# Kernel optimization log

Hardware: AMD Instinct MI355X
Metric: run time of the kernel (lower is better)

Reference implementation:

```python
import jax, jax.numpy as jnp
import numpy as np

B, H, W = 16, 256, 256
C = 64          # width
M1, M2 = 12, 12 # retained Fourier modes
FC_HID = 128


def setup_inputs() -> dict:
    key = jax.random.key(0)
    ks = jax.random.split(key, 10)
    scale = 1.0 / (C * C)
    inp = {
        "x": jax.random.normal(ks[0], (B, H, W, 1), dtype=jnp.float32),
        "fc0_w": jax.random.normal(ks[1], (1, C), dtype=jnp.float32) * (1.0 / np.sqrt(1)),
        "fc0_b": jnp.zeros((C,), dtype=jnp.float32),
        # 4 layers x {weights1, weights2} x [Cin, Cout, M1, M2] x {re, im}
        "sc_w": jax.random.uniform(ks[2], (4, 2, C, C, M1, M2, 2), dtype=jnp.float32) * scale,
        # 1x1 conv weights [layer, Cout, Cin] and biases [layer, Cout]
        "pw_w": jax.random.normal(ks[3], (4, C, C), dtype=jnp.float32) * (1.0 / np.sqrt(C)),
        "pw_b": jnp.zeros((4, C), dtype=jnp.float32),
        "fc1_w": jax.random.normal(ks[4], (C, FC_HID), dtype=jnp.float32) * (1.0 / np.sqrt(C)),
        "fc1_b": jnp.zeros((FC_HID,), dtype=jnp.float32),
        "fc2_w": jax.random.normal(ks[5], (FC_HID, 1), dtype=jnp.float32) * (1.0 / np.sqrt(FC_HID)),
        "fc2_b": jnp.zeros((1,), dtype=jnp.float32),
    }
    return inp


def _spectral_conv(x, w1, w2):
    # x: [B, C, H, W] real; w1, w2: [Cin, Cout, M1, M2] complex
    xf = jnp.fft.rfft2(x, axes=(-2, -1))                # [B, C, H, W//2+1]
    top = jnp.einsum('bixy,ioxy->boxy', xf[:, :, :M1, :M2], w1)
    bot = jnp.einsum('bixy,ioxy->boxy', xf[:, :, -M1:, :M2], w2)
    out_ft = jnp.zeros((x.shape[0], w1.shape[1], x.shape[2], x.shape[3] // 2 + 1),
                       dtype=jnp.complex64)
    out_ft = out_ft.at[:, :, :M1, :M2].set(top)
    out_ft = out_ft.at[:, :, -M1:, :M2].set(bot)
    return jnp.fft.irfft2(out_ft, s=(x.shape[2], x.shape[3]), axes=(-2, -1))


def _gelu(x):
    return jax.nn.gelu(x, approximate=False)  # torch F.gelu default = exact erf


def reference(x, fc0_w, fc0_b, sc_w, pw_w, pw_b, fc1_w, fc1_b, fc2_w, fc2_b):
    # lift: [B,H,W,1] -> [B,H,W,C] -> [B,C,H,W]
    h = jnp.einsum('bhwi,ic->bhwc', x, fc0_w) + fc0_b
    h = jnp.transpose(h, (0, 3, 1, 2))
    scw = sc_w[..., 0] + 1j * sc_w[..., 1]  # [4, 2, C, C, M1, M2] complex
    for l in range(4):
        x1 = _spectral_conv(h, scw[l, 0], scw[l, 1])
        x2 = jnp.einsum('bihw,oi->bohw', h, pw_w[l]) + pw_b[l][None, :, None, None]
        h = x1 + x2
        if l < 3:
            h = _gelu(h)
    h = jnp.transpose(h, (0, 2, 3, 1))  # [B,H,W,C]
    h = _gelu(jnp.einsum('bhwc,cd->bhwd', h, fc1_w) + fc1_b)
    out = jnp.einsum('bhwd,do->bhwo', h, fc2_w) + fc2_b
    return out
```

## Files before the change

### kernel.cpp

```cpp
#include <hip/hip_runtime.h>
#include <hip/hip_bf16.h>
#include <math.h>

#define Hn 256
#define Wn 256
#define Cn 64
#define Mk 12
#define NM 24
#define FCH 128
#define HW 65536

using half8 = __attribute__((ext_vector_type(8))) _Float16;
using f32x4 = __attribute__((ext_vector_type(4))) float;

__device__ __forceinline__ float gelu_exact(float x) {
    return 0.5f * x * (1.0f + erff(x * 0.7071067811865476f));
}
__device__ __forceinline__ unsigned short f2h(float f) {
    _Float16 h = (_Float16)f;
    return __builtin_bit_cast(unsigned short, h);
}

__global__ __launch_bounds__(256) void k_init_tables(float* tc, float* ts,
                                                     float* twc, float* tws,
                                                     float* tcs,
                                                     unsigned short* bfr,
                                                     unsigned short* tfr) {
    int i = threadIdx.x;
    const float step = 0.024543692606170259f;
    float c = cosf(i * step), s = sinf(i * step);
    tc[i] = c; ts[i] = s;
    tcs[2 * i] = c; tcs[2 * i + 1] = s;
    for (int k = 0; k < Mk; ++k) {
        int idx = (i * k) & 255;
        twc[i * Mk + k] = cosf(idx * step);
        tws[i * Mk + k] = sinf(idx * step);
    }
    for (int e = i; e < 8192; e += 256) {
        int j  = e & 7;
        int l  = (e >> 3) & 63;
        int sn = e >> 9;
        int col = (sn & 1) * 16 + (l & 15);
        int ky = col >> 1, p = col & 1;
        int k  = (sn >> 1) * 32 + ((l >> 4) & 3) * 8 + j;
        int idx = (ky * k) & 255;
        float v = p ? -sinf(idx * step) : cosf(idx * step);
        bfr[e] = f2h(v);
    }
    for (int e = i; e < 12288; e += 256) {
        int j  = e & 7;
        int l  = (e >> 3) & 63;
        int sm = e >> 9;
        int mt = sm % 3, s2 = sm / 3;
        int r  = mt * 16 + (l & 15);
        int hh = s2 * 32 + ((l >> 4) & 3) * 8 + j;
        int m  = (r < 24) ? r : (r - 24);
        int kx = (m < Mk) ? m : (232 + m);
        int idx = (kx * hh) & 255;
        float v = (r < 24) ? cosf(idx * step) : sinf(idx * step);
        tfr[e] = f2h(v);
    }
}

__global__ __launch_bounds__(256) void k_prep_frag(const float* __restrict__ pww,
                                                   const float* __restrict__ fc1w,
                                                   unsigned short* __restrict__ efr,
                                                   unsigned short* __restrict__ pwfr,
                                                   unsigned short* __restrict__ fc1fr) {
    int e = blockIdx.x * 256 + threadIdx.x;
    const float step = 0.024543692606170259f;
    int j = e & 7, l = (e >> 3) & 63;
    int row = l & 15;
    int k = ((l >> 4) & 3) * 8 + j;
    if (e < 8192) {
        int mt = (e >> 9) & 15;
        int pix = mt * 16 + row;
        float v = 0.f;
        if (k < 12) v = cosf(((k * pix) & 255) * step);
        else if (k < 24) v = -sinf((((k - 12) * pix) & 255) * step);
        efr[e] = f2h(v);
    } else if (e < 24576) {
        int e2 = e - 8192;
        int nt = (e2 >> 9) & 3;
        int ks = (e2 >> 11) & 1;
        int l4 = e2 >> 12;
        int o = nt * 16 + row;
        int i = ks * 32 + k;
        pwfr[e2] = f2h(pww[(size_t)(l4 * 64 + o) * 64 + i]);
    } else {
        int e2 = e - 24576;
        int nt = (e2 >> 9) & 7;
        int ks = (e2 >> 12) & 1;
        int d = nt * 16 + row;
        int i = ks * 32 + k;
        fc1fr[e2] = f2h(fc1w[i * 128 + d]);
    }
}

__global__ __launch_bounds__(256) void k_prep_w(const float* __restrict__ scw,
                                                float* __restrict__ scwT) {
    int t = blockIdx.x * 256 + threadIdx.x;
    int o  = t & 63;
    int i  = (t >> 6) & 63;
    int r  = t >> 12;
    int u  = r % 6;
    int kx = (r / 6) % 12;
    int lj = r / 72;
    int ky = 2 * u;
    size_t in_idx = ((((size_t)lj * 64 + i) * 64 + o) * 144) + kx * Mk + ky;
    float4 v = *(const float4*)(scw + 2 * in_idx);
    size_t o0 = ((((size_t)(lj * 12 + kx) * Mk + ky) * 64 + i) * 64 + o);
    size_t o1 = ((((size_t)(lj * 12 + kx) * Mk + ky + 1) * 64 + i) * 64 + o);
    *(float2*)(scwT + 2 * o0) = make_float2(v.x, v.y);
    *(float2*)(scwT + 2 * o1) = make_float2(v.z, v.w);
}

__global__ __launch_bounds__(64) void k_dftw_x(const float* __restrict__ x,
                                               float* __restrict__ Xxw,
                                               const float* __restrict__ twc,
                                               const float* __restrict__ tws) {
    int r = blockIdx.x * 64 + threadIdx.x;
    const float* hp = x + (size_t)r * Wn;
    float xr[Mk], xi[Mk];
#pragma unroll
    for (int k = 0; k < Mk; ++k) { xr[k] = 0.f; xi[k] = 0.f; }
    for (int w4 = 0; w4 < 64; ++w4) {
        float4 v = ((const float4*)hp)[w4];
        float vv[4] = {v.x, v.y, v.z, v.w};
#pragma unroll
        for (int j = 0; j < 4; ++j) {
            int wbase = (w4 * 4 + j) * Mk;
#pragma unroll
            for (int k = 0; k < Mk; ++k) {
                xr[k] += vv[j] * twc[wbase + k];
                xi[k] -= vv[j] * tws[wbase + k];
            }
        }
    }
    float* op = Xxw + (size_t)r * (2 * Mk);
#pragma unroll
    for (int k = 0; k < Mk; ++k) { op[2 * k] = xr[k]; op[2 * k + 1] = xi[k]; }
}

__global__ __launch_bounds__(256) void k_xdfth(const float* __restrict__ Xxw,
                                               float* __restrict__ Xfx,
                                               const float* __restrict__ tc,
                                               const float* __restrict__ ts) {
    int t = blockIdx.x * 256 + threadIdx.x;
    if (t >= 16 * 288) return;
    int ky = t % Mk;
    int m  = (t / Mk) % NM;
    int b  = t / 288;
    int kx = (m < Mk) ? m : (232 + m);
    const float* base = Xxw + (size_t)b * Hn * 2 * Mk + 2 * ky;
    float ar = 0.f, ai = 0.f;
    for (int hh = 0; hh < Hn; ++hh) {
        float vr = base[hh * 2 * Mk];
        float vi = base[hh * 2 * Mk + 1];
        int idx = (kx * hh) & 255;
        float c = tc[idx], s = ts[idx];
        ar += vr * c + vi * s;
        ai += vi * c - vr * s;
    }
    Xfx[2 * t] = ar;
    Xfx[2 * t + 1] = ai;
}

__global__ __launch_bounds__(256, 2) void k_mix0(const float* __restrict__ Xfx,
                                                 const float* __restrict__ scwT,
                                                 const float* __restrict__ w0,
                                                 const float* __restrict__ b0v,
                                                 float* __restrict__ Z, int b0) {
    __shared__ float red[512];
    int blk = blockIdx.x;
    int b = blk / 288, mk = blk % 288;
    int m = mk / Mk, ky = mk % Mk;
    int t = threadIdx.x;
    int o = t & 63, q = t >> 6;
    float xr = Xfx[((b0 + b) * 288 + mk) * 2];
    float xi = Xfx[((b0 + b) * 288 + mk) * 2 + 1];
    int j = (m < Mk) ? 0 : 1;
    int kxw = (m < Mk) ? m : (m - Mk);
    const float* wb = scwT + ((size_t)((j * Mk + kxw) * Mk + ky) * 4096 + (q * 16) * 64 + o) * 2;
    float zr = 0.f, zi = 0.f;
#pragma unroll
    for (int ii = 0; ii < 16; ++ii) {
        int i = q * 16 + ii;
        float ar = w0[i] * xr, ai = w0[i] * xi;
        if (mk == 0) ar += 65536.0f * b0v[i];
        float wr = wb[ii * 128], wi = wb[ii * 128 + 1];
        zr += ar * wr - ai * wi;
        zi += ar * wi + ai * wr;
    }
    red[t * 2] = zr; red[t * 2 + 1] = zi;
    __syncthreads();
    if (t < 64) {
        float sr = red[t * 2] + red[(t + 64) * 2] + red[(t + 128) * 2] + red[(t + 192) * 2];
        float si = red[t * 2 + 1] + red[(t + 64) * 2 + 1] + red[(t + 128) * 2 + 1] + red[(t + 192) * 2 + 1];
        const float sc = 2.0f / 65536.0f;
        float2* zo = (float2*)Z + (((size_t)b * Mk + ky) * 64 + t) * 24 + m;
        *zo = make_float2(sr * sc, si * sc);
    }
}

__global__ __launch_bounds__(256) void k_dfth(const float* __restrict__ Xw,
                                              float* __restrict__ Xf2,
                                              const unsigned short* __restrict__ tfr) {
    __shared__ __align__(16) char smem[65536];
    int b = blockIdx.x / 12, ky = blockIdx.x % 12;
    int t = threadIdx.x;
    int lane = t & 63, q = t >> 6;
    const float* P = Xw + ((size_t)b * 12 + ky) * 32768;
    int c = lane;
#pragma unroll 4
    for (int k = 0; k < 32; ++k) {
        int hh0 = k * 8 + q * 2;
        float2 a  = *(const float2*)(P + hh0 * 128 + 2 * c);
        float2 bv = *(const float2*)(P + (hh0 + 1) * 128 + 2 * c);
        unsigned int u0 = f2h(a.x * 0.0625f) | ((unsigned int)f2h(bv.x * 0.0625f) << 16);
        unsigned int u1 = f2h(a.y * 0.0625f) | ((unsigned int)f2h(bv.y * 0.0625f) << 16);
        int ch0 = 2 * c, ch1 = 2 * c + 1;
        *(unsigned int*)(smem + ch0 * 512 + ((2 * hh0) ^ ((ch0 & 7) << 4))) = u0;
        *(unsigned int*)(smem + ch1 * 512 + ((2 * hh0) ^ ((ch1 & 7) << 4))) = u1;
    }
    __syncthreads();
    int ct0 = q * 2;
    int tg = (lane >> 4) & 3;
    f32x4 a00 = {0,0,0,0}, a01 = {0,0,0,0}, a10 = {0,0,0,0};
    f32x4 a11 = {0,0,0,0}, a20 = {0,0,0,0}, a21 = {0,0,0,0};
    const uint4* tf4 = (const uint4*)tfr;
#pragma unroll
    for (int s = 0; s < 8; ++s) {
        half8 af0 = __builtin_bit_cast(half8, tf4[(s * 3 + 0) * 64 + lane]);
        half8 af1 = __builtin_bit_cast(half8, tf4[(s * 3 + 1) * 64 + lane]);
        half8 af2 = __builtin_bit_cast(half8, tf4[(s * 3 + 2) * 64 + lane]);
        int chan0 = ct0 * 16 + (lane & 15);
        int chan1 = chan0 + 16;
        int off = s * 64 + tg * 16;
        half8 b0 = *(const half8*)(smem + chan0 * 512 + (off ^ ((chan0 & 7) << 4)));
        half8 b1 = *(const half8*)(smem + chan1 * 512 + (off ^ ((chan1 & 7) << 4)));
        a00 = __builtin_amdgcn_mfma_f32_16x16x32_f16(af0, b0, a00, 0, 0, 0);
        a01 = __builtin_amdgcn_mfma_f32_16x16x32_f16(af0, b1, a01, 0, 0, 0);
        a10 = __builtin_amdgcn_mfma_f32_16x16x32_f16(af1, b0, a10, 0, 0, 0);
        a11 = __builtin_amdgcn_mfma_f32_16x16x32_f16(af1, b1, a11, 0, 0, 0);
        a20 = __builtin_amdgcn_mfma_f32_16x16x32_f16(af2, b0, a20, 0, 0, 0);
        a21 = __builtin_amdgcn_mfma_f32_16x16x32_f16(af2, b1, a21, 0, 0, 0);
    }
    __syncthreads();
    float* Cs = (float*)smem;
    {
        int rl = (lane >> 4) * 4;
        int chan0 = ct0 * 16 + (lane & 15);
#pragma unroll
        for (int r = 0; r < 4; ++r) {
            Cs[(0  + rl + r) * 128 + chan0]      = a00[r];
            Cs[(0  + rl + r) * 128 + chan0 + 16] = a01[r];
            Cs[(16 + rl + r) * 128 + chan0]      = a10[r];
            Cs[(16 + rl + r) * 128 + chan0 + 16] = a11[r];
            Cs[(32 + rl + r) * 128 + chan0]      = a20[r];
            Cs[(32 + rl + r) * 128 + chan0 + 16] = a21[r];
        }
    }
    __syncthreads();
#pragma unroll
    for (int k = 0; k < 6; ++k) {
        int p = t + 256 * k;
        int m = p >> 6, i = p & 63;
        float r1 = Cs[m * 128 + 2 * i];
        float i1 = Cs[m * 128 + 2 * i + 1];
        float r2 = Cs[(24 + m) * 128 + 2 * i];
        float i2 = Cs[(24 + m) * 128 + 2 * i + 1];
        ((float2*)Xf2)[((size_t)b * 288 + m * 12 + ky) * 64 + i] =
            make_float2((r1 + i2) * 16.0f, (i1 - r2) * 16.0f);
    }
}

__global__ __launch_bounds__(256, 2) void k_mixZ(const float* __restrict__ Xf2,
                                                 const float* __restrict__ scwT,
                                                 float* __restrict__ Z, int l) {
    __shared__ float red[512];
    __shared__ float xf[128];
    int blk = blockIdx.x;
    int b = blk / 288, mk = blk % 288;
    int m = mk / Mk, ky = mk % Mk;
    int t = threadIdx.x;
    if (t < 64) {
        float2 v = ((const float2*)Xf2)[((size_t)b * 288 + mk) * 64 + t];
        xf[2 * t] = v.x; xf[2 * t + 1] = v.y;
    }
    __syncthreads();
    int o = t & 63, q = t >> 6;
    int j = (m < Mk) ? 0 : 1;
    int kxw = (m < Mk) ? m : (m - Mk);
    const float* wb = scwT + ((size_t)(((l * 2 + j) * Mk + kxw) * Mk + ky) * 4096 + (q * 16) * 64 + o) * 2;
    float zr = 0.f, zi = 0.f;
#pragma unroll
    for (int ii = 0; ii < 16; ++ii) {
        float br = xf[(q * 16 + ii) * 2], bi = xf[(q * 16 + ii) * 2 + 1];
        float wr = wb[ii * 128], wi = wb[ii * 128 + 1];
        zr += br * wr - bi * wi;
        zi += br * wi + bi * wr;
    }
    __syncthreads();
    red[t * 2] = zr; red[t * 2 + 1] = zi;
    __syncthreads();
    if (t < 64) {
        float sr = red[t * 2] + red[(t + 64) * 2] + red[(t + 128) * 2] + red[(t + 192) * 2];
        float si = red[t * 2 + 1] + red[(t + 64) * 2 + 1] + red[(t + 128) * 2 + 1] + red[(t + 192) * 2 + 1];
        const float sc = 2.0f / 65536.0f;
        float2* zo = (float2*)Z + (((size_t)b * Mk + ky) * 64 + t) * 24 + m;
        *zo = make_float2(sr * sc, si * sc);
    }
}

__global__ __launch_bounds__(256) void k_fusedA(const float* xh,
        const float* __restrict__ Zb, const float* __restrict__ pwb,
        const float* __restrict__ w0, const float* __restrict__ b0v,
        float* hn, float* __restrict__ XwOut,
        const float* __restrict__ tcs,
        const unsigned short* __restrict__ bfr,
        const unsigned short* __restrict__ efr,
        const unsigned short* __restrict__ pwfr,
        int l, int first) {
    __shared__ __align__(16) char smem[37120];
    float* Ysh = (float*)smem;
    char*  Yfr = smem + 32768;
    float* csm = (float*)(smem + 36864);
    int b  = blockIdx.x >> 8;
    int hh = blockIdx.x & 255;
    int w  = threadIdx.x;
    int lane = w & 63, q = w >> 6;
    int tg = (lane >> 4) & 3;
    const float2* tc2 = (const float2*)tcs;
    if (w < NM) {
        int kx = (w < Mk) ? w : (232 + w);
        float2 cs = tc2[(kx * hh) & 255];
        csm[2 * w] = cs.x; csm[2 * w + 1] = cs.y;
    }
    __syncthreads();
    const float* Zbb = Zb + (size_t)b * 36864;
    const float4* cs4 = (const float4*)csm;
#pragma unroll
    for (int r3 = 0; r3 < 3; ++r3) {
        int p = w + 256 * r3;
        int o = p / Mk, ky = p % Mk;
        const float4* zv = (const float4*)(Zbb + ((size_t)ky * 64 + o) * 48);
        float yr = 0.f, yi = 0.f;
#pragma unroll
        for (int mm = 0; mm < 12; ++mm) {
            float4 z  = zv[mm];
            float4 cc = cs4[mm];
            yr += z.x * cc.x - z.y * cc.y + z.z * cc.z - z.w * cc.w;
            yi += z.x * cc.y + z.y * cc.x + z.z * cc.w + z.w * cc.z;
        }
        Ysh[p * 2] = yr; Ysh[p * 2 + 1] = yi;
    }
    __syncthreads();
    {
        int o = q * 16 + (lane & 15);
        unsigned pv[4];
#pragma unroll
        for (int jp = 0; jp < 4; ++jp) {
            unsigned short h2[2];
#pragma unroll
            for (int hzz = 0; hzz < 2; ++hzz) {
                int u = tg * 8 + jp * 2 + hzz;
                float v;
                if (u == 0) v = 0.5f * Ysh[o * 24];
                else if (u < 12) v = Ysh[o * 24 + 2 * u];
                else if (u < 24) v = Ysh[o * 24 + 2 * (u - 12) + 1];
                else v = 0.f;
                h2[hzz] = f2h(v);
            }
            pv[jp] = h2[0] | ((unsigned)h2[1] << 16);
        }
        uint4 pk = {pv[0], pv[1], pv[2], pv[3]};
        *(uint4*)(Yfr + (q * 64 + lane) * 16) = pk;
    }
    __syncthreads();
    {
        int swz = (w & 7) << 4;
        if (first) {
            float xv = xh[(size_t)b * HW + hh * 256 + w];
#pragma unroll
            for (int ic = 0; ic < 4; ++ic) {
                unsigned pv[8];
#pragma unroll
                for (int j2 = 0; j2 < 16; j2 += 2) {
                    float a0 = w0[ic * 16 + j2] * xv + b0v[ic * 16 + j2];
                    float a1 = w0[ic * 16 + j2 + 1] * xv + b0v[ic * 16 + j2 + 1];
                    pv[j2 >> 1] = f2h(a0) | ((unsigned)f2h(a1) << 16);
                }
                uint4 lo = {pv[0], pv[1], pv[2], pv[3]};
                uint4 hi = {pv[4], pv[5], pv[6], pv[7]};
                *(uint4*)(smem + ((w * 128 + ic * 32) ^ swz)) = lo;
                *(uint4*)(smem + ((w * 128 + ic * 32 + 16) ^ swz)) = hi;
            }
        } else {
            const float* hb = xh + (size_t)b * Cn * HW + hh * 256 + w;
#pragma unroll
            for (int ic = 0; ic < 4; ++ic) {
                unsigned pv[8];
#pragma unroll
                for (int j2 = 0; j2 < 16; j2 += 2) {
                    float a0 = hb[(size_t)(ic * 16 + j2) * HW];
                    float a1 = hb[(size_t)(ic * 16 + j2 + 1) * HW];
                    pv[j2 >> 1] = f2h(a0) | ((unsigned)f2h(a1) << 16);
                }
                uint4 lo = {pv[0], pv[1], pv[2], pv[3]};
                uint4 hi = {pv[4], pv[5], pv[6], pv[7]};
                *(uint4*)(smem + ((w * 128 + ic * 32) ^ swz)) = lo;
                *(uint4*)(smem + ((w * 128 + ic * 32 + 16) ^ swz)) = hi;
            }
        }
    }
    __syncthreads();
    float g[4][4][4];
    {
        const uint4* efr4 = (const uint4*)efr;
        const uint4* pw4  = (const uint4*)pwfr;
        float biasn[4];
        half8 ybf[4]; uint4 cwa[4], cwb[4];
#pragma unroll
        for (int nt = 0; nt < 4; ++nt) {
            biasn[nt] = pwb[l * 64 + nt * 16 + (lane & 15)];
            ybf[nt] = *(const half8*)(Yfr + (nt * 64 + lane) * 16);
            cwa[nt] = pw4[((l * 2 + 0) * 4 + nt) * 64 + lane];
            cwb[nt] = pw4[((l * 2 + 1) * 4 + nt) * 64 + lane];
        }
#pragma unroll
        for (int mt = 0; mt < 4; ++mt) {
            int mtA = q * 4 + mt;
            half8 ea = __builtin_bit_cast(half8, efr4[mtA * 64 + lane]);
            int row = mtA * 16 + (lane & 15);
            int rsw = (row & 7) << 4;
            half8 a0 = *(const half8*)(smem + ((row * 128 + tg * 16) ^ rsw));
            half8 a1 = *(const half8*)(smem + ((row * 128 + 64 + tg * 16) ^ rsw));
#pragma unroll
            for (int nt = 0; nt < 4; ++nt) {
                f32x4 acc = {0.f, 0.f, 0.f, 0.f};
                acc = __builtin_amdgcn_mfma_f32_16x16x32_f16(ea, ybf[nt], acc, 0, 0, 0);
                acc = __builtin_amdgcn_mfma_f32_16x16x32_f16(a0, __builtin_bit_cast(half8, cwa[nt]), acc, 0, 0, 0);
                acc = __builtin_amdgcn_mfma_f32_16x16x32_f16(a1, __builtin_bit_cast(half8, cwb[nt]), acc, 0, 0, 0);
#pragma unroll
                for (int r = 0; r < 4; ++r)
                    g[mt][nt][r] = gelu_exact(acc[r] + biasn[nt]);
            }
        }
    }
    float* hnb = hn + (size_t)b * Cn * HW + hh * 256;
#pragma unroll
    for (int mt = 0; mt < 4; ++mt) {
        int pbase = (q * 4 + mt) * 16 + (lane >> 4) * 4;
#pragma unroll
        for (int nt = 0; nt < 4; ++nt) {
            int o = nt * 16 + (lane & 15);
            float4 hv = {g[mt][nt][0], g[mt][nt][1], g[mt][nt][2], g[mt][nt][3]};
            *(float4*)(hnb + (size_t)o * HW + pbase) = hv;
        }
    }
    __syncthreads();
#pragma unroll
    for (int mt = 0; mt < 4; ++mt) {
        int pbase = (q * 4 + mt) * 16 + (lane >> 4) * 4;
#pragma unroll
        for (int nt = 0; nt < 4; ++nt) {
            int o = nt * 16 + (lane & 15);
            int sidx = (((pbase >> 3) ^ (o & 7)) << 3) | (pbase & 7);
            uint2 pk2;
            pk2.x = f2h(g[mt][nt][0]) | ((unsigned)f2h(g[mt][nt][1]) << 16);
            pk2.y = f2h(g[mt][nt][2]) | ((unsigned)f2h(g[mt][nt][3]) << 16);
            *(uint2*)(smem + o * 512 + sidx * 2) = pk2;
        }
    }
    __syncthreads();
    {
        int arow = q * 16 + (lane & 15);
        const uint4* bt = (const uint4*)bfr;
        f32x4 ac0 = {0.f, 0.f, 0.f, 0.f};
        f32x4 ac1 = {0.f, 0.f, 0.f, 0.f};
#pragma unroll
        for (int s = 0; s < 8; ++s) {
            int abyte = (arow * 512 + s * 64 + tg * 16) ^ ((arow & 7) << 4);
            half8 af = __builtin_bit_cast(half8, *(const uint4*)(smem + abyte));
            half8 b0 = __builtin_bit_cast(half8, bt[(s * 2 + 0) * 64 + lane]);
            half8 b1 = __builtin_bit_cast(half8, bt[(s * 2 + 1) * 64 + lane]);
            ac0 = __builtin_amdgcn_mfma_f32_16x16x32_f16(af, b0, ac0, 0, 0, 0);
            ac1 = __builtin_amdgcn_mfma_f32_16x16x32_f16(af, b1, ac1, 0, 0, 0);
        }
        float* Xwb = XwOut + (size_t)b * 393216;
        int rbase = q * 16 + (lane >> 4) * 4;
#pragma unroll
        for (int n = 0; n < 2; ++n) {
            f32x4 ac = n ? ac1 : ac0;
            int col = n * 16 + (lane & 15);
            int ky = col >> 1, p = col & 1;
            if (ky < Mk) {
                float* dst = Xwb + (size_t)ky * 32768 + hh * 128 + rbase * 2 + p;
                dst[0] = ac[0]; dst[2] = ac[1]; dst[4] = ac[2]; dst[6] = ac[3];
            }
        }
    }
}

__global__ __launch_bounds__(256) void k_fusedB(const float* __restrict__ h,
        const float* __restrict__ Zb, const float* __restrict__ pwb,
        const float* __restrict__ fc1b, const float* __restrict__ fc2w,
        const float* __restrict__ fc2b, float* __restrict__ outp,
        const float* __restrict__ tcs,
        const unsigned short* __restrict__ efr,
        const unsigned short* __restrict__ pwfr,
        const unsigned short* __restrict__ fc1fr) {
    __shared__ __align__(16) char smem[37120];
    float* Ysh = (float*)smem;
    char*  Yfr = smem + 32768;
    float* csm = (float*)(smem + 36864);
    int b  = blockIdx.x >> 8;
    int hh = blockIdx.x & 255;
    int w  = threadIdx.x;
    int lane = w & 63, q = w >> 6;
    int tg = (lane >> 4) & 3;
    const float2* tc2 = (const float2*)tcs;
    if (w < NM) {
        int kx = (w < Mk) ? w : (232 + w);
        float2 cs = tc2[(kx * hh) & 255];
        csm[2 * w] = cs.x; csm[2 * w + 1] = cs.y;
    }
    __syncthreads();
    const float* Zbb = Zb + (size_t)b * 36864;
    const float4* cs4 = (const float4*)csm;
#pragma unroll
    for (int r3 = 0; r3 < 3; ++r3) {
        int p = w + 256 * r3;
        int o = p / Mk, ky = p % Mk;
        const float4* zv = (const float4*)(Zbb + ((size_t)ky * 64 + o) * 48);
        float yr = 0.f, yi = 0.f;
#pragma unroll
        for (int mm = 0; mm < 12; ++mm) {
            float4 z  = zv[mm];
            float4 cc = cs4[mm];
            yr += z.x * cc.x - z.y * cc.y + z.z * cc.z - z.w * cc.w;
            yi += z.x * cc.y + z.y * cc.x + z.z * cc.w + z.w * cc.z;
        }
        Ysh[p * 2] = yr; Ysh[p * 2 + 1] = yi;
    }
    __syncthreads();
    {
        int o = q * 16 + (lane & 15);
        unsigned pv[4];
#pragma unroll
        for (int jp = 0; jp < 4; ++jp) {
            unsigned short h2[2];
#pragma unroll
            for (int hzz = 0; hzz < 2; ++hzz) {
                int u = tg * 8 + jp * 2 + hzz;
                float v;
                if (u == 0) v = 0.5f * Ysh[o * 24];
                else if (u < 12) v = Ysh[o * 24 + 2 * u];
                else if (u < 24) v = Ysh[o * 24 + 2 * (u - 12) + 1];
                else v = 0.f;
                h2[hzz] = f2h(v);
            }
            pv[jp] = h2[0] | ((unsigned)h2[1] << 16);
        }
        uint4 pk = {pv[0], pv[1], pv[2], pv[3]};
        *(uint4*)(Yfr + (q * 64 + lane) * 16) = pk;
    }
    __syncthreads();
    {
        int swz = (w & 7) << 4;
        const float* hb = h + (size_t)b * Cn * HW + hh * 256 + w;
#pragma unroll
        for (int ic = 0; ic < 4; ++ic) {
            unsigned pv[8];
#pragma unroll
            for (int j2 = 0; j2 < 16; j2 += 2) {
                float a0 = hb[(size_t)(ic * 16 + j2) * HW];
                float a1 = hb[(size_t)(ic * 16 + j2 + 1) * HW];
                pv[j2 >> 1] = f2h(a0) | ((unsigned)f2h(a1) << 16);
            }
            uint4 lo = {pv[0], pv[1], pv[2], pv[3]};
            uint4 hi = {pv[4], pv[5], pv[6], pv[7]};
            *(uint4*)(smem + ((w * 128 + ic * 32) ^ swz)) = lo;
            *(uint4*)(smem + ((w * 128 + ic * 32 + 16) ^ swz)) = hi;
        }
    }
    __syncthreads();
    float R[16][4];
    {
        const uint4* efr4 = (const uint4*)efr;
        const uint4* pw4 = (const uint4*)pwfr;
        half8 ay  = *(const half8*)(Yfr + (q * 64 + lane) * 16);
        half8 aw0 = __builtin_bit_cast(half8, pw4[((3 * 2 + 0) * 4 + q) * 64 + lane]);
        half8 aw1 = __builtin_bit_cast(half8, pw4[((3 * 2 + 1) * 4 + q) * 64 + lane]);
        int obase = q * 16 + (lane >> 4) * 4;
        float4 bias4 = *(const float4*)(pwb + 3 * 64 + obase);
#pragma unroll
        for (int nt = 0; nt < 16; ++nt) {
            half8 eb = __builtin_bit_cast(half8, efr4[nt * 64 + lane]);
            int pix = nt * 16 + (lane & 15);
            int psw = (pix & 7) << 4;
            half8 b0 = *(const half8*)(smem + ((pix * 128 + tg * 16) ^ psw));
            half8 b1 = *(const half8*)(smem + ((pix * 128 + 64 + tg * 16) ^ psw));
            f32x4 acc = {0.f, 0.f, 0.f, 0.f};
            acc = __builtin_amdgcn_mfma_f32_16x16x32_f16(ay, eb, acc, 0, 0, 0);
            acc = __builtin_amdgcn_mfma_f32_16x16x32_f16(aw0, b0, acc, 0, 0, 0);
            acc = __builtin_amdgcn_mfma_f32_16x16x32_f16(aw1, b1, acc, 0, 0, 0);
            R[nt][0] = acc[0] + bias4.x; R[nt][1] = acc[1] + bias4.y;
            R[nt][2] = acc[2] + bias4.z; R[nt][3] = acc[3] + bias4.w;
        }
    }
    __syncthreads();
    {
        int obase = q * 16 + (lane >> 4) * 4;
#pragma unroll
        for (int nt = 0; nt < 16; ++nt) {
            int pix = nt * 16 + (lane & 15);
            uint2 pk2;
            pk2.x = f2h(R[nt][0]) | ((unsigned)f2h(R[nt][1]) << 16);
            pk2.y = f2h(R[nt][2]) | ((unsigned)f2h(R[nt][3]) << 16);
            *(uint2*)(smem + ((pix * 128 + obase * 2) ^ ((pix & 7) << 4))) = pk2;
        }
    }
    __syncthreads();
    const uint4* f14 = (const uint4*)fc1fr;
    float w2v[8], fb1[8];
#pragma unroll
    for (int nt = 0; nt < 8; ++nt) {
        w2v[nt] = fc2w[nt * 16 + (lane & 15)];
        fb1[nt] = fc1b[nt * 16 + (lane & 15)];
    }
    float fb = fc2b[0];
    float* ob = outp + (size_t)b * HW + hh * 256;
#pragma unroll
    for (int mt = 0; mt < 4; ++mt) {
        int mtA = q * 4 + mt;
        int row = mtA * 16 + (lane & 15);
        int rsw = (row & 7) << 4;
        half8 a0 = *(const half8*)(smem + ((row * 128 + tg * 16) ^ rsw));
        half8 a1 = *(const half8*)(smem + ((row * 128 + 64 + tg * 16) ^ rsw));
        float s0 = 0.f, s1 = 0.f, s2 = 0.f, s3 = 0.f;
#pragma unroll
        for (int nt = 0; nt < 8; ++nt) {
            f32x4 acc = {0.f, 0.f, 0.f, 0.f};
            acc = __builtin_amdgcn_mfma_f32_16x16x32_f16(a0, __builtin_bit_cast(half8, f14[(0 * 8 + nt) * 64 + lane]), acc, 0, 0, 0);
            acc = __builtin_amdgcn_mfma_f32_16x16x32_f16(a1, __builtin_bit_cast(half8, f14[(1 * 8 + nt) * 64 + lane]), acc, 0, 0, 0);
            s0 += gelu_exact(acc[0] + fb1[nt]) * w2v[nt];
            s1 += gelu_exact(acc[1] + fb1[nt]) * w2v[nt];
            s2 += gelu_exact(acc[2] + fb1[nt]) * w2v[nt];
            s3 += gelu_exact(acc[3] + fb1[nt]) * w2v[nt];
        }
#pragma unroll
        for (int msk = 1; msk <= 8; msk <<= 1) {
            s0 += __shfl_xor(s0, msk);
            s1 += __shfl_xor(s1, msk);
            s2 += __shfl_xor(s2, msk);
            s3 += __shfl_xor(s3, msk);
        }
        int cc = lane & 15;
        if (cc < 4) {
            float v = (cc == 0) ? s0 : (cc == 1) ? s1 : (cc == 2) ? s2 : s3;
            ob[mtA * 16 + (lane >> 4) * 4 + cc] = v + fb;
        }
    }
}

extern "C" void kernel_launch(void* const* d_in, const int* in_sizes, int n_in,
                              void* d_out, int out_size, void* d_ws, size_t ws_size,
                              hipStream_t stream) {
    const float* x    = (const float*)d_in[0];
    const float* fc0w = (const float*)d_in[1];
    const float* fc0b = (const float*)d_in[2];
    const float* scw  = (const float*)d_in[3];
    const float* pww  = (const float*)d_in[4];
    const float* pwb  = (const float*)d_in[5];
    const float* fc1w = (const float*)d_in[6];
    const float* fc1b = (const float*)d_in[7];
    const float* fc2w = (const float*)d_in[8];
    const float* fc2b = (const float*)d_in[9];
    float* out = (float*)d_out;
    float* ws  = (float*)d_ws;

    const size_t basef = 9480192;
    const size_t perbf = 4661248;
    int bc = 0;
    for (int cand = 16; cand >= 1; cand >>= 1)
        if ((basef + perbf * (size_t)cand) * 4 <= ws_size) { bc = cand; break; }
    if (bc == 0) return;

    float* tabc = ws;
    float* tabs = tabc + 256;
    float* twc  = tabs + 256;
    float* tws_ = twc + 3072;
    float* tcs  = tws_ + 3072;
    float* bfr  = tcs + 512;
    float* tfr  = bfr + 4096;
    float* efr  = tfr + 6144;
    float* pwfr = efr + 4096;
    float* fc1f = pwfr + 8192;
    float* Xfx  = fc1f + 4096;
    float* scwT = Xfx + 9216;
    float* hbuf = ws + basef;
    float* Xw   = hbuf + (size_t)bc * 4194304;
    float* Zb   = Xw + (size_t)bc * 393216;
    float* Xf2  = Zb + (size_t)bc * 36864;

    k_init_tables<<<1, 256, 0, stream>>>(tabc, tabs, twc, tws_, tcs,
                                         (unsigned short*)bfr,
                                         (unsigned short*)tfr);
    k_prep_frag<<<128, 256, 0, stream>>>(pww, fc1w,
                                         (unsigned short*)efr,
                                         (unsigned short*)pwfr,
                                         (unsigned short*)fc1f);
    k_prep_w<<<9216, 256, 0, stream>>>(scw, scwT);
    k_dftw_x<<<64, 64, 0, stream>>>(x, hbuf, twc, tws_);
    k_xdfth<<<18, 256, 0, stream>>>(hbuf, Xfx, tabc, tabs);

    for (int b0 = 0; b0 < 16; b0 += bc) {
        k_mix0<<<bc * 288, 256, 0, stream>>>(Xfx, scwT, fc0w, fc0b, Zb, b0);
        k_fusedA<<<bc * 256, 256, 0, stream>>>(x + (size_t)b0 * HW, Zb, pwb,
                                               fc0w, fc0b, hbuf, Xw, tcs,
                                               (const unsigned short*)bfr,
                                               (const unsigned short*)efr,
                                               (const unsigned short*)pwfr, 0, 1);
        for (int l = 1; l <= 2; ++l) {
            k_dfth<<<bc * 12, 256, 0, stream>>>(Xw, Xf2, (const unsigned short*)tfr);
            k_mixZ<<<bc * 288, 256, 0, stream>>>(Xf2, scwT, Zb, l);
            k_fusedA<<<bc * 256, 256, 0, stream>>>(hbuf, Zb, pwb,
                                                   fc0w, fc0b, hbuf, Xw, tcs,
                                                   (const unsigned short*)bfr,
                                                   (const unsigned short*)efr,
                                                   (const unsigned short*)pwfr, l, 0);
        }
        k_dfth<<<bc * 12, 256, 0, stream>>>(Xw, Xf2, (const unsigned short*)tfr);
        k_mixZ<<<bc * 288, 256, 0, stream>>>(Xf2, scwT, Zb, 3);
        k_fusedB<<<bc * 256, 256, 0, stream>>>(hbuf, Zb, pwb, fc1b, fc2w, fc2b,
                                               out + (size_t)b0 * HW, tcs,
                                               (const unsigned short*)efr,
                                               (const unsigned short*)pwfr,
                                               (const unsigned short*)fc1f);
    }
}
```

Before: 1.327 ms.

## Run spectral mode mixing as batched fp16 MFMA GEMM with prepacked weights

Replaces the scalar per-(batch,mode) complex mixing kernels with one kernel per mode that batches all samples as the M dimension of 16x16x32 fp16 MFMAs. Complex weights are expanded once into real 2x2 block fragments in fp16 by a new prep kernel. Each weight matrix is then read once per layer instead of once per batch sample. The fused kernels also keep GELU and pre-activation results packed as fp16 to cut register pressure, and request 4 blocks per CU. This adds fp16 rounding to the spectral weights and inputs, and enlarges the workspace.

```diff
diff --git a/kernel.cpp b/kernel.cpp
--- a/kernel.cpp
+++ b/kernel.cpp
@@ -19,6 +19,12 @@
 __device__ __forceinline__ unsigned short f2h(float f) {
     _Float16 h = (_Float16)f;
     return __builtin_bit_cast(unsigned short, h);
+}
+__device__ __forceinline__ float h2lo(unsigned u) {
+    return (float)__builtin_bit_cast(_Float16, (unsigned short)(u & 0xffffu));
+}
+__device__ __forceinline__ float h2hi(unsigned u) {
+    return (float)__builtin_bit_cast(_Float16, (unsigned short)(u >> 16));
 }
 
 __global__ __launch_bounds__(256) void k_init_tables(float* tc, float* ts,
@@ -115,6 +121,45 @@
     *(float2*)(scwT + 2 * o1) = make_float2(v.z, v.w);
 }
 
+__global__ __launch_bounds__(256) void k_prep_wfrag(const float* __restrict__ scwT,
+                                                    unsigned short* __restrict__ wfr) {
+    __shared__ float Ws[8192];
+    int mat = blockIdx.x;
+    int t = threadIdx.x;
+    const float4* src = (const float4*)(scwT + (size_t)mat * 8192);
+#pragma unroll
+    for (int r = 0; r < 8; ++r)
+        ((float4*)Ws)[r * 256 + t] = src[r * 256 + t];
+    __syncthreads();
+    unsigned short* dst = wfr + (size_t)mat * 16384;
+#pragma unroll
+    for (int u = 0; u < 8; ++u) {
+        int lin = u * 256 + t;
+        int lane = lin & 63, nt = (lin >> 6) & 7, s = lin >> 9;
+        int col = nt * 16 + (lane & 15);
+        int o = col >> 1, pp = col & 1;
+        int tg = (lane >> 4) & 3;
+        unsigned pk[4];
+#pragma unroll
+        for (int jp = 0; jp < 4; ++jp) {
+            unsigned short hv[2];
+#pragma unroll
+            for (int hz = 0; hz < 2; ++hz) {
+                int k = s * 32 + tg * 8 + jp * 2 + hz;
+                int i = k >> 1, p = k & 1;
+                float wr_ = Ws[(i * 64 + o) * 2];
+                float wi_ = Ws[(i * 64 + o) * 2 + 1];
+                float v = (p == 0) ? (pp == 0 ? wr_ : wi_)
+                                   : (pp == 0 ? -wi_ : wr_);
+                hv[hz] = f2h(v);
+            }
+            pk[jp] = hv[0] | ((unsigned)hv[1] << 16);
+        }
+        uint4 w4 = {pk[0], pk[1], pk[2], pk[3]};
+        *(uint4*)(dst + lin * 8) = w4;
+    }
+}
+
 __global__ __launch_bounds__(64) void k_dftw_x(const float* __restrict__ x,
                                                float* __restrict__ Xxw,
                                                const float* __restrict__ twc,
@@ -166,40 +211,75 @@
     Xfx[2 * t + 1] = ai;
 }
 
-__global__ __launch_bounds__(256, 2) void k_mix0(const float* __restrict__ Xfx,
-                                                 const float* __restrict__ scwT,
-                                                 const float* __restrict__ w0,
-                                                 const float* __restrict__ b0v,
-                                                 float* __restrict__ Z, int b0) {
-    __shared__ float red[512];
+__global__ __launch_bounds__(256) void k_mixZ2(const float* __restrict__ xin,
+                                               const unsigned short* __restrict__ wfr,
+                                               const float* __restrict__ w0,
+                                               const float* __restrict__ b0v,
+                                               float* __restrict__ Z,
+                                               int l, int first, int b0, int bc) {
+    __shared__ __align__(16) char smem[4096];
+    int t = threadIdx.x;
+    int lane = t & 63, q = t >> 6, tg = (lane >> 4) & 3;
     int blk = blockIdx.x;
-    int b = blk / 288, mk = blk % 288;
-    int m = mk / Mk, ky = mk % Mk;
-    int t = threadIdx.x;
-    int o = t & 63, q = t >> 6;
-    float xr = Xfx[((b0 + b) * 288 + mk) * 2];
-    float xi = Xfx[((b0 + b) * 288 + mk) * 2 + 1];
-    int j = (m < Mk) ? 0 : 1;
-    int kxw = (m < Mk) ? m : (m - Mk);
-    const float* wb = scwT + ((size_t)((j * Mk + kxw) * Mk + ky) * 4096 + (q * 16) * 64 + o) * 2;
-    float zr = 0.f, zi = 0.f;
-#pragma unroll
-    for (int ii = 0; ii < 16; ++ii) {
-        int i = q * 16 + ii;
-        float ar = w0[i] * xr, ai = w0[i] * xi;
-        if (mk == 0) ar += 65536.0f * b0v[i];
-        float wr = wb[ii * 128], wi = wb[ii * 128 + 1];
-        zr += ar * wr - ai * wi;
-        zi += ar * wi + ai * wr;
-    }
-    red[t * 2] = zr; red[t * 2 + 1] = zi;
-    __syncthreads();
-    if (t < 64) {
-        float sr = red[t * 2] + red[(t + 64) * 2] + red[(t + 128) * 2] + red[(t + 192) * 2];
-        float si = red[t * 2 + 1] + red[(t + 64) * 2 + 1] + red[(t + 128) * 2 + 1] + red[(t + 192) * 2 + 1];
-        const float sc = 2.0f / 65536.0f;
-        float2* zo = (float2*)Z + (((size_t)b * Mk + ky) * 64 + t) * 24 + m;
-        *zo = make_float2(sr * sc, si * sc);
+    int jj = blk / 144, kxw = (blk / 12) % 12, ky = blk % 12;
+    int mm = jj * 12 + kxw;
+    int mk = mm * 12 + ky;
+    int mat = (l * 2 + jj) * 144 + kxw * 12 + ky;
+    {
+        int b = t >> 4, c16 = t & 15;
+        uint4 pk = {0u, 0u, 0u, 0u};
+        if (b < bc) {
+            if (first) {
+                float xr = xin[((b0 + b) * 288 + mk) * 2] * 0.0625f;
+                float xi = xin[((b0 + b) * 288 + mk) * 2 + 1] * 0.0625f;
+                float4 wv = *(const float4*)(w0 + c16 * 4);
+                float4 bv = {0.f, 0.f, 0.f, 0.f};
+                if (mk == 0) {
+                    float4 bb = *(const float4*)(b0v + c16 * 4);
+                    bv.x = 4096.f * bb.x; bv.y = 4096.f * bb.y;
+                    bv.z = 4096.f * bb.z; bv.w = 4096.f * bb.w;
+                }
+                pk.x = f2h(wv.x * xr + bv.x) | ((unsigned)f2h(wv.x * xi) << 16);
+                pk.y = f2h(wv.y * xr + bv.y) | ((unsigned)f2h(wv.y * xi) << 16);
+                pk.z = f2h(wv.z * xr + bv.z) | ((unsigned)f2h(wv.z * xi) << 16);
+                pk.w = f2h(wv.w * xr + bv.w) | ((unsigned)f2h(wv.w * xi) << 16);
+            } else {
+                const float* src = xin + ((size_t)b * 288 + mk) * 128 + c16 * 8;
+                float4 v0 = *(const float4*)(src);
+                float4 v1 = *(const float4*)(src + 4);
+                pk.x = f2h(v0.x * 0.0625f) | ((unsigned)f2h(v0.y * 0.0625f) << 16);
+                pk.y = f2h(v0.z * 0.0625f) | ((unsigned)f2h(v0.w * 0.0625f) << 16);
+                pk.z = f2h(v1.x * 0.0625f) | ((unsigned)f2h(v1.y * 0.0625f) << 16);
+                pk.w = f2h(v1.z * 0.0625f) | ((unsigned)f2h(v1.w * 0.0625f) << 16);
+            }
+        }
+        *(uint4*)(smem + ((b * 256 + c16 * 16) ^ ((b & 7) << 4))) = pk;
+    }
+    __syncthreads();
+    const uint4* bt = (const uint4*)wfr + (size_t)mat * 2048;
+    f32x4 ac0 = {0.f, 0.f, 0.f, 0.f};
+    f32x4 ac1 = {0.f, 0.f, 0.f, 0.f};
+    int brow = lane & 15;
+#pragma unroll
+    for (int s = 0; s < 4; ++s) {
+        half8 af = *(const half8*)(smem + ((brow * 256 + s * 64 + tg * 16) ^ ((brow & 7) << 4)));
+        half8 bf0 = __builtin_bit_cast(half8, bt[(s * 8 + 2 * q) * 64 + lane]);
+        half8 bf1 = __builtin_bit_cast(half8, bt[(s * 8 + 2 * q + 1) * 64 + lane]);
+        ac0 = __builtin_amdgcn_mfma_f32_16x16x32_f16(af, bf0, ac0, 0, 0, 0);
+        ac1 = __builtin_amdgcn_mfma_f32_16x16x32_f16(af, bf1, ac1, 0, 0, 0);
+    }
+    const float sc = 16.0f * 2.0f / 65536.0f;
+#pragma unroll
+    for (int n = 0; n < 2; ++n) {
+        f32x4 ac = n ? ac1 : ac0;
+        int col = (2 * q + n) * 16 + (lane & 15);
+        int o = col >> 1, pp = col & 1;
+#pragma unroll
+        for (int r = 0; r < 4; ++r) {
+            int bb = (lane >> 4) * 4 + r;
+            if (bb < bc)
+                Z[(((size_t)bb * 12 + ky) * 64 + o) * 48 + mm * 2 + pp] = ac[r] * sc;
+        }
     }
 }
 
@@ -275,45 +355,7 @@
     }
 }
 
-__global__ __launch_bounds__(256, 2) void k_mixZ(const float* __restrict__ Xf2,
-                                                 const float* __restrict__ scwT,
-                                                 float* __restrict__ Z, int l) {
-    __shared__ float red[512];
-    __shared__ float xf[128];
-    int blk = blockIdx.x;
-    int b = blk / 288, mk = blk % 288;
-    int m = mk / Mk, ky = mk % Mk;
-    int t = threadIdx.x;
-    if (t < 64) {
-        float2 v = ((const float2*)Xf2)[((size_t)b * 288 + mk) * 64 + t];
-        xf[2 * t] = v.x; xf[2 * t + 1] = v.y;
-    }
-    __syncthreads();
-    int o = t & 63, q = t >> 6;
-    int j = (m < Mk) ? 0 : 1;
-    int kxw = (m < Mk) ? m : (m - Mk);
-    const float* wb = scwT + ((size_t)(((l * 2 + j) * Mk + kxw) * Mk + ky) * 4096 + (q * 16) * 64 + o) * 2;
-    float zr = 0.f, zi = 0.f;
-#pragma unroll
-    for (int ii = 0; ii < 16; ++ii) {
-        float br = xf[(q * 16 + ii) * 2], bi = xf[(q * 16 + ii) * 2 + 1];
-        float wr = wb[ii * 128], wi = wb[ii * 128 + 1];
-        zr += br * wr - bi * wi;
-        zi += br * wi + bi * wr;
-    }
-    __syncthreads();
-    red[t * 2] = zr; red[t * 2 + 1] = zi;
-    __syncthreads();
-    if (t < 64) {
-        float sr = red[t * 2] + red[(t + 64) * 2] + red[(t + 128) * 2] + red[(t + 192) * 2];
-        float si = red[t * 2 + 1] + red[(t + 64) * 2 + 1] + red[(t + 128) * 2 + 1] + red[(t + 192) * 2 + 1];
-        const float sc = 2.0f / 65536.0f;
-        float2* zo = (float2*)Z + (((size_t)b * Mk + ky) * 64 + t) * 24 + m;
-        *zo = make_float2(sr * sc, si * sc);
-    }
-}
-
-__global__ __launch_bounds__(256) void k_fusedA(const float* xh,
+__global__ __launch_bounds__(256, 4) void k_fusedA(const float* xh,
         const float* __restrict__ Zb, const float* __restrict__ pwb,
         const float* __restrict__ w0, const float* __restrict__ b0v,
         float* hn, float* __restrict__ XwOut,
@@ -415,7 +457,7 @@
         }
     }
     __syncthreads();
-    float g[4][4][4];
+    uint2 gp[4][4];
     {
         const uint4* efr4 = (const uint4*)efr;
         const uint4* pw4  = (const uint4*)pwfr;
@@ -442,9 +484,12 @@
                 acc = __builtin_amdgcn_mfma_f32_16x16x32_f16(ea, ybf[nt], acc, 0, 0, 0);
                 acc = __builtin_amdgcn_mfma_f32_16x16x32_f16(a0, __builtin_bit_cast(half8, cwa[nt]), acc, 0, 0, 0);
                 acc = __builtin_amdgcn_mfma_f32_16x16x32_f16(a1, __builtin_bit_cast(half8, cwb[nt]), acc, 0, 0, 0);
-#pragma unroll
-                for (int r = 0; r < 4; ++r)
-                    g[mt][nt][r] = gelu_exact(acc[r] + biasn[nt]);
+                float g0 = gelu_exact(acc[0] + biasn[nt]);
+                float g1 = gelu_exact(acc[1] + biasn[nt]);
+                float g2 = gelu_exact(acc[2] + biasn[nt]);
+                float g3 = gelu_exact(acc[3] + biasn[nt]);
+                gp[mt][nt].x = f2h(g0) | ((unsigned)f2h(g1) << 16);
+                gp[mt][nt].y = f2h(g2) | ((unsigned)f2h(g3) << 16);
             }
         }
     }
@@ -455,7 +500,8 @@
 #pragma unroll
         for (int nt = 0; nt < 4; ++nt) {
             int o = nt * 16 + (lane & 15);
-            float4 hv = {g[mt][nt][0], g[mt][nt][1], g[mt][nt][2], g[mt][nt][3]};
+            uint2 g2 = gp[mt][nt];
+            float4 hv = {h2lo(g2.x), h2hi(g2.x), h2lo(g2.y), h2hi(g2.y)};
             *(float4*)(hnb + (size_t)o * HW + pbase) = hv;
         }
     }
@@ -467,10 +513,7 @@
         for (int nt = 0; nt < 4; ++nt) {
             int o = nt * 16 + (lane & 15);
             int sidx = (((pbase >> 3) ^ (o & 7)) << 3) | (pbase & 7);
-            uint2 pk2;
-            pk2.x = f2h(g[mt][nt][0]) | ((unsigned)f2h(g[mt][nt][1]) << 16);
-            pk2.y = f2h(g[mt][nt][2]) | ((unsigned)f2h(g[mt][nt][3]) << 16);
-            *(uint2*)(smem + o * 512 + sidx * 2) = pk2;
+            *(uint2*)(smem + o * 512 + sidx * 2) = gp[mt][nt];
         }
     }
     __syncthreads();
@@ -503,7 +546,7 @@
     }
 }
 
-__global__ __launch_bounds__(256) void k_fusedB(const float* __restrict__ h,
+__global__ __launch_bounds__(256, 4) void k_fusedB(const float* __restrict__ h,
         const float* __restrict__ Zb, const float* __restrict__ pwb,
         const float* __restrict__ fc1b, const float* __restrict__ fc2w,
         const float* __restrict__ fc2b, float* __restrict__ outp,
@@ -586,7 +629,7 @@
         }
     }
     __syncthreads();
-    float R[16][4];
+    uint2 R2[16];
     {
         const uint4* efr4 = (const uint4*)efr;
         const uint4* pw4 = (const uint4*)pwfr;
@@ -606,8 +649,8 @@
             acc = __builtin_amdgcn_mfma_f32_16x16x32_f16(ay, eb, acc, 0, 0, 0);
             acc = __builtin_amdgcn_mfma_f32_16x16x32_f16(aw0, b0, acc, 0, 0, 0);
             acc = __builtin_amdgcn_mfma_f32_16x16x32_f16(aw1, b1, acc, 0, 0, 0);
-            R[nt][0] = acc[0] + bias4.x; R[nt][1] = acc[1] + bias4.y;
-            R[nt][2] = acc[2] + bias4.z; R[nt][3] = acc[3] + bias4.w;
+            R2[nt].x = f2h(acc[0] + bias4.x) | ((unsigned)f2h(acc[1] + bias4.y) << 16);
+            R2[nt].y = f2h(acc[2] + bias4.z) | ((unsigned)f2h(acc[3] + bias4.w) << 16);
         }
     }
     __syncthreads();
@@ -616,10 +659,7 @@
 #pragma unroll
         for (int nt = 0; nt < 16; ++nt) {
             int pix = nt * 16 + (lane & 15);
-            uint2 pk2;
-            pk2.x = f2h(R[nt][0]) | ((unsigned)f2h(R[nt][1]) << 16);
-            pk2.y = f2h(R[nt][2]) | ((unsigned)f2h(R[nt][3]) << 16);
-            *(uint2*)(smem + ((pix * 128 + obase * 2) ^ ((pix & 7) << 4))) = pk2;
+            *(uint2*)(smem + ((pix * 128 + obase * 2) ^ ((pix & 7) << 4))) = R2[nt];
         }
     }
     __syncthreads();
@@ -681,7 +721,7 @@
     float* out = (float*)d_out;
     float* ws  = (float*)d_ws;
 
-    const size_t basef = 9480192;
+    const size_t basef = 18917376;
     const size_t perbf = 4661248;
     int bc = 0;
     for (int cand = 16; cand >= 1; cand >>= 1)
@@ -700,6 +740,7 @@
     float* fc1f = pwfr + 8192;
     float* Xfx  = fc1f + 4096;
     float* scwT = Xfx + 9216;
+    float* wfr  = scwT + 9437184;
     float* hbuf = ws + basef;
     float* Xw   = hbuf + (size_t)bc * 4194304;
     float* Zb   = Xw + (size_t)bc * 393216;
@@ -713,11 +754,13 @@
                                          (unsigned short*)pwfr,
                                          (unsigned short*)fc1f);
     k_prep_w<<<9216, 256, 0, stream>>>(scw, scwT);
+    k_prep_wfrag<<<1152, 256, 0, stream>>>(scwT, (unsigned short*)wfr);
     k_dftw_x<<<64, 64, 0, stream>>>(x, hbuf, twc, tws_);
     k_xdfth<<<18, 256, 0, stream>>>(hbuf, Xfx, tabc, tabs);
 
     for (int b0 = 0; b0 < 16; b0 += bc) {
-        k_mix0<<<bc * 288, 256, 0, stream>>>(Xfx, scwT, fc0w, fc0b, Zb, b0);
+        k_mixZ2<<<288, 256, 0, stream>>>(Xfx, (const unsigned short*)wfr,
+                                         fc0w, fc0b, Zb, 0, 1, b0, bc);
         k_fusedA<<<bc * 256, 256, 0, stream>>>(x + (size_t)b0 * HW, Zb, pwb,
                                                fc0w, fc0b, hbuf, Xw, tcs,
                                                (const unsigned short*)bfr,
@@ -725,7 +768,8 @@
                                                (const unsigned short*)pwfr, 0, 1);
         for (int l = 1; l <= 2; ++l) {
             k_dfth<<<bc * 12, 256, 0, stream>>>(Xw, Xf2, (const unsigned short*)tfr);
-            k_mixZ<<<bc * 288, 256, 0, stream>>>(Xf2, scwT, Zb, l);
+            k_mixZ2<<<288, 256, 0, stream>>>(Xf2, (const unsigned short*)wfr,
+                                             fc0w, fc0b, Zb, l, 0, b0, bc);
             k_fusedA<<<bc * 256, 256, 0, stream>>>(hbuf, Zb, pwb,
                                                    fc0w, fc0b, hbuf, Xw, tcs,
                                                    (const unsigned short*)bfr,
@@ -733,7 +777,8 @@
                                                    (const unsigned short*)pwfr, l, 0);
         }
         k_dfth<<<bc * 12, 256, 0, stream>>>(Xw, Xf2, (const unsigned short*)tfr);
-        k_mixZ<<<bc * 288, 256, 0, stream>>>(Xf2, scwT, Zb, 3);
+        k_mixZ2<<<288, 256, 0, stream>>>(Xf2, (const unsigned short*)wfr,
+                                         fc0w, fc0b, Zb, 3, 0, b0, bc);
         k_fusedB<<<bc * 256, 256, 0, stream>>>(hbuf, Zb, pwb, fc1b, fc2w, fc2b,
                                                out + (size_t)b0 * HW, tcs,
                                                (const unsigned short*)efr,
```

Result: slower. 1.605 ms (+20.9%).
